# Kernel tuning notes

Measured on AMD Instinct MI355X. Metric: run time of the kernel, lower is better.

The kernel has to match this reference:

```python
import jax, jax.numpy as jnp
import numpy as np

B, T, I, H, O = 256, 512, 128, 256, 1


def setup_inputs() -> dict:
    key = jax.random.key(0)
    ks = jax.random.split(key, 7)
    s_ih = 1.0 / np.sqrt(H)
    return {
        "x": jax.random.normal(ks[0], (B, T, I), dtype=jnp.float32),
        "W_ih": jax.random.uniform(ks[1], (H, I), jnp.float32, -s_ih, s_ih),
        "W_hh": jax.random.uniform(ks[2], (H, H), jnp.float32, -s_ih, s_ih),
        "b_ih": jax.random.uniform(ks[3], (H,), jnp.float32, -s_ih, s_ih),
        "b_hh": jax.random.uniform(ks[4], (H,), jnp.float32, -s_ih, s_ih),
        "fc_w": jax.random.uniform(ks[5], (O, H), jnp.float32, -s_ih, s_ih),
        "fc_b": jax.random.uniform(ks[6], (O,), jnp.float32, -s_ih, s_ih),
    }


def reference(x, W_ih, W_hh, b_ih, b_hh, fc_w, fc_b):
    # Elman RNN (tanh), batch_first, single layer, h0 = zeros.
    # Only the last hidden state feeds the fc head, so scan carries h only.
    b = b_ih + b_hh
    xW = jnp.einsum('bti,hi->tbh', x, W_ih) + b  # precompute input projection [T,B,H]

    def step(h, xw_t):
        h = jnp.tanh(xw_t + h @ W_hh.T)
        return h, None

    h0 = jnp.zeros((x.shape[0], W_hh.shape[0]), dtype=x.dtype)
    h_last, _ = jax.lax.scan(step, h0, xW)
    return h_last @ fc_w.T + fc_b  # [B, O]
```

## Files before the change

kernel.cpp:

```cpp
#include <hip/hip_runtime.h>
#include <hip/hip_bf16.h>

#define B_ 256
#define T_ 512
#define I_ 128
#define H_ 256

typedef __bf16 bf16x8 __attribute__((ext_vector_type(8)));
typedef float  f32x4  __attribute__((ext_vector_type(4)));
typedef unsigned short u16;
typedef unsigned int   u32;

union U16x8Cast { uint4 v; bf16x8 b; };

__device__ inline u16 f2b(float f) {
    union { __bf16 h; u16 u; } c; c.h = (__bf16)f; return c.u;
}
__device__ inline bf16x8 pack8(float4 lo, float4 hi) {
    bf16x8 f;
    f[0]=(__bf16)lo.x; f[1]=(__bf16)lo.y; f[2]=(__bf16)lo.z; f[3]=(__bf16)lo.w;
    f[4]=(__bf16)hi.x; f[5]=(__bf16)hi.y; f[6]=(__bf16)hi.z; f[7]=(__bf16)hi.w;
    return f;
}
__device__ inline uint2 pack4(float a, float b, float c, float d) {
    uint2 p;
    p.x = (u32)f2b(a) | ((u32)f2b(b) << 16);
    p.y = (u32)f2b(c) | ((u32)f2b(d) << 16);
    return p;
}
__device__ inline f32x4 b4_to_f32x4(uint2 u) {
    f32x4 r;
    r[0] = __uint_as_float(u.x << 16);
    r[1] = __uint_as_float(u.x & 0xFFFF0000u);
    r[2] = __uint_as_float(u.y << 16);
    r[3] = __uint_as_float(u.y & 0xFFFF0000u);
    return r;
}
__device__ inline float fast_tanh(float x) {
    float e = __expf(2.f * x);
    float d = 1.f + e;
    float r;
    asm("v_rcp_f32 %0, %1" : "=v"(r) : "v"(d));
    return fmaf(-2.f, r, 1.f);
}

#define WG_BARRIER() asm volatile("s_waitcnt lgkmcnt(0)\n\ts_barrier" ::: "memory")

#define LDST 264
__global__ __launch_bounds__(256, 2) void xw_gemm_mfma(const float* __restrict__ x,
                                                       const float* __restrict__ W_ih,
                                                       const float* __restrict__ b_ih,
                                                       const float* __restrict__ b_hh,
                                                       u16* __restrict__ xw) {
    __shared__ u16 tile[64 * LDST];

    const int tid  = (int)threadIdx.x;
    const int wave = tid >> 6;
    const int lane = tid & 63;
    const int q    = lane >> 4;
    const int ml   = lane & 15;
    const int m0   = (int)blockIdx.x * 128;
    const int b    = m0 >> 9;
    const int t0   = m0 & 511;
    const int n0   = wave * 64;

    bf16x8 wA[4][4];
#pragma unroll
    for (int tau = 0; tau < 4; ++tau) {
        const float* wr = W_ih + (size_t)(n0 + tau * 16 + ml) * I_;
#pragma unroll
        for (int kap = 0; kap < 4; ++kap) {
            const int k0 = kap * 32 + q * 8;
            wA[tau][kap] = pack8(*(const float4*)(wr + k0), *(const float4*)(wr + k0 + 4));
        }
    }

    f32x4 acc[8][4];
#pragma unroll
    for (int mt = 0; mt < 8; ++mt)
#pragma unroll
        for (int tau = 0; tau < 4; ++tau) acc[mt][tau] = (f32x4)0.f;

#pragma unroll
    for (int kap = 0; kap < 4; ++kap) {
        bf16x8 xB[8];
#pragma unroll
        for (int mt = 0; mt < 8; ++mt) {
            const float* xr = x + (size_t)(m0 + mt * 16 + ml) * I_ + kap * 32 + q * 8;
            xB[mt] = pack8(*(const float4*)xr, *(const float4*)(xr + 4));
        }
#pragma unroll
        for (int mt = 0; mt < 8; ++mt)
#pragma unroll
            for (int tau = 0; tau < 4; ++tau)
                acc[mt][tau] = __builtin_amdgcn_mfma_f32_16x16x32_bf16(
                    wA[tau][kap], xB[mt], acc[mt][tau], 0, 0, 0);
    }

    float4 bias4[4];
#pragma unroll
    for (int tau = 0; tau < 4; ++tau) {
        const int n = n0 + tau * 16 + q * 4;
        float4 bi = *(const float4*)(b_ih + n);
        float4 bh = *(const float4*)(b_hh + n);
        bias4[tau] = make_float4(bi.x + bh.x, bi.y + bh.y, bi.z + bh.z, bi.w + bh.w);
    }

#pragma unroll
    for (int p = 0; p < 2; ++p) {
        if (p) __syncthreads();
#pragma unroll
        for (int mt = 0; mt < 4; ++mt) {
            const int row = mt * 16 + ml;
            const int mg  = p * 4 + mt;
#pragma unroll
            for (int tau = 0; tau < 4; ++tau) {
                uint2 pk = pack4(acc[mg][tau][0] + bias4[tau].x,
                                 acc[mg][tau][1] + bias4[tau].y,
                                 acc[mg][tau][2] + bias4[tau].z,
                                 acc[mg][tau][3] + bias4[tau].w);
                *(uint2*)(tile + row * LDST + n0 + tau * 16 + q * 4) = pk;
            }
        }
        __syncthreads();
#pragma unroll
        for (int s = 0; s < 4; ++s) {
            const int rr = s * 16 + (tid >> 4);
            const int c  = tid & 15;
            const uint4* srcp = (const uint4*)(tile + rr * LDST);
            uint4* dstp = (uint4*)(xw + ((size_t)(t0 + p * 64 + rr) * B_ + b) * H_);
            uint4 v0 = srcp[c];
            uint4 v1 = srcp[c + 16];
            dstp[c] = v0;
            dstp[c + 16] = v1;
        }
    }
}

__global__ __launch_bounds__(512, 2) void rnn_scan_mfma(const u16* __restrict__ xw,
                                                        const float* __restrict__ W_hh,
                                                        const float* __restrict__ fc_w,
                                                        const float* __restrict__ fc_b,
                                                        float* __restrict__ out) {
    __shared__ __attribute__((aligned(16))) u16 hbuf[2][4096];
    __shared__ float red[8][16];

    const int tid  = (int)threadIdx.x;
    const int wave = tid >> 6;
    const int lane = tid & 63;
    const int q    = lane >> 4;
    const int m    = lane & 15;
    const int b0   = (int)blockIdx.x * 16;

    bf16x8 wf[2][8];
#pragma unroll
    for (int tau2 = 0; tau2 < 2; ++tau2) {
        const float* wr = W_hh + (size_t)(wave * 32 + tau2 * 16 + m) * H_;
#pragma unroll
        for (int kap = 0; kap < 8; ++kap) {
            const int k0 = kap * 32 + q * 8;
            wf[tau2][kap] = pack8(*(const float4*)(wr + k0), *(const float4*)(wr + k0 + 4));
        }
    }

    int widx[2];
#pragma unroll
    for (int tau2 = 0; tau2 < 2; ++tau2) {
        const int nbw = wave * 32 + tau2 * 16 + q * 4;
        widx[tau2] = (nbw >> 5) * 512 + (((nbw >> 3) & 3) * 16 + m) * 8 + (nbw & 7);
    }

    {
        uint4* p = (uint4*)&hbuf[0][0];
        const uint4 z = {0u, 0u, 0u, 0u};
        p[tid] = z;
    }
    WG_BARRIER();

    const u16* xwp = xw + (size_t)(b0 + m) * H_ + (wave * 32 + q * 4);
    const size_t tstride = (size_t)B_ * H_;

    uint2 pfA[2], pfB[2];
    pfA[0] = *(const uint2*)(xwp);
    pfA[1] = *(const uint2*)(xwp + 16);
    pfB[0] = *(const uint2*)(xwp + tstride);
    pfB[1] = *(const uint2*)(xwp + tstride + 16);

    int cur = 0;
    f32x4 acc[2];
    for (int tt = 0; tt < T_ / 2; ++tt) {
        {
            const int t = 2 * tt;
            acc[0] = b4_to_f32x4(pfA[0]);
            acc[1] = b4_to_f32x4(pfA[1]);
            if (t + 2 < T_) {
                const u16* pt = xwp + (size_t)(t + 2) * tstride;
                pfA[0] = *(const uint2*)(pt);
                pfA[1] = *(const uint2*)(pt + 16);
            }
            const uint4* hb = (const uint4*)&hbuf[cur][0];
#pragma unroll
            for (int kap = 0; kap < 8; ++kap) {
                U16x8Cast c; c.v = hb[kap * 64 + lane];
                acc[0] = __builtin_amdgcn_mfma_f32_16x16x32_bf16(wf[0][kap], c.b, acc[0], 0, 0, 0);
                acc[1] = __builtin_amdgcn_mfma_f32_16x16x32_bf16(wf[1][kap], c.b, acc[1], 0, 0, 0);
            }
            u16* wb = &hbuf[cur ^ 1][0];
#pragma unroll
            for (int tau2 = 0; tau2 < 2; ++tau2) {
                uint2 pk = pack4(fast_tanh(acc[tau2][0]), fast_tanh(acc[tau2][1]),
                                 fast_tanh(acc[tau2][2]), fast_tanh(acc[tau2][3]));
                *(uint2*)(wb + widx[tau2]) = pk;
            }
            WG_BARRIER();
            cur ^= 1;
        }
        {
            const int t = 2 * tt + 1;
            acc[0] = b4_to_f32x4(pfB[0]);
            acc[1] = b4_to_f32x4(pfB[1]);
            if (t + 2 < T_) {
                const u16* pt = xwp + (size_t)(t + 2) * tstride;
                pfB[0] = *(const uint2*)(pt);
                pfB[1] = *(const uint2*)(pt + 16);
            }
            const uint4* hb = (const uint4*)&hbuf[cur][0];
#pragma unroll
            for (int kap = 0; kap < 8; ++kap) {
                U16x8Cast c; c.v = hb[kap * 64 + lane];
                acc[0] = __builtin_amdgcn_mfma_f32_16x16x32_bf16(wf[0][kap], c.b, acc[0], 0, 0, 0);
                acc[1] = __builtin_amdgcn_mfma_f32_16x16x32_bf16(wf[1][kap], c.b, acc[1], 0, 0, 0);
            }
            if (t != T_ - 1) {
                u16* wb = &hbuf[cur ^ 1][0];
#pragma unroll
                for (int tau2 = 0; tau2 < 2; ++tau2) {
                    uint2 pk = pack4(fast_tanh(acc[tau2][0]), fast_tanh(acc[tau2][1]),
                                     fast_tanh(acc[tau2][2]), fast_tanh(acc[tau2][3]));
                    *(uint2*)(wb + widx[tau2]) = pk;
                }
                WG_BARRIER();
                cur ^= 1;
            }
        }
    }

    float4 fcw[2];
#pragma unroll
    for (int tau2 = 0; tau2 < 2; ++tau2)
        fcw[tau2] = *(const float4*)(fc_w + wave * 32 + tau2 * 16 + q * 4);

    float partial = 0.f;
#pragma unroll
    for (int tau2 = 0; tau2 < 2; ++tau2) {
        partial += fast_tanh(acc[tau2][0]) * fcw[tau2].x;
        partial += fast_tanh(acc[tau2][1]) * fcw[tau2].y;
        partial += fast_tanh(acc[tau2][2]) * fcw[tau2].z;
        partial += fast_tanh(acc[tau2][3]) * fcw[tau2].w;
    }
    partial += __shfl_xor(partial, 16);
    partial += __shfl_xor(partial, 32);
    __syncthreads();
    if (lane < 16) red[wave][m] = partial;
    __syncthreads();
    if (tid < 16) {
        float s = red[0][tid] + red[1][tid] + red[2][tid] + red[3][tid]
                + red[4][tid] + red[5][tid] + red[6][tid] + red[7][tid];
        out[b0 + tid] = s + fc_b[0];
    }
}

extern "C" void kernel_launch(void* const* d_in, const int* in_sizes, int n_in,
                              void* d_out, int out_size, void* d_ws, size_t ws_size,
                              hipStream_t stream) {
    const float* x    = (const float*)d_in[0];
    const float* W_ih = (const float*)d_in[1];
    const float* W_hh = (const float*)d_in[2];
    const float* b_ih = (const float*)d_in[3];
    const float* b_hh = (const float*)d_in[4];
    const float* fc_w = (const float*)d_in[5];
    const float* fc_b = (const float*)d_in[6];
    float* out = (float*)d_out;

    u16* xwbuf = (u16*)d_ws;
    xw_gemm_mfma<<<(B_ * T_) / 128, 256, 0, stream>>>(x, W_ih, b_ih, b_hh, xwbuf);
    rnn_scan_mfma<<<B_ / 16, 512, 0, stream>>>(xwbuf, W_hh, fc_w, fc_b, out);
}
```

Measured before the change: 457.9 us.

## Halve scan workgroup to 4 waves, each computing 64 hidden units

The recurrent scan kernel now uses 256 threads (4 waves) per 16-batch block instead of 512, and each wave owns 64 hidden outputs with four accumulator tiles and four W_hh fragment sets held in registers. This cuts the per-step barrier cost and the number of waves synchronising, and gives each wave more independent MFMA chains to hide latency. In exchange each wave does twice the MFMA and tanh work per step on the serial critical path, and register pressure roughly doubles.

Result: slower. 531.3 us (+16.0%).

```diff
diff --git a/kernel.cpp b/kernel.cpp
--- a/kernel.cpp
+++ b/kernel.cpp
@@ -137,13 +137,13 @@
     }
 }
 
-__global__ __launch_bounds__(512, 2) void rnn_scan_mfma(const u16* __restrict__ xw,
+__global__ __launch_bounds__(256, 1) void rnn_scan_mfma(const u16* __restrict__ xw,
                                                         const float* __restrict__ W_hh,
                                                         const float* __restrict__ fc_w,
                                                         const float* __restrict__ fc_b,
                                                         float* __restrict__ out) {
     __shared__ __attribute__((aligned(16))) u16 hbuf[2][4096];
-    __shared__ float red[8][16];
+    __shared__ float red[4][16];
 
     const int tid  = (int)threadIdx.x;
     const int wave = tid >> 6;
@@ -152,92 +152,97 @@
     const int m    = lane & 15;
     const int b0   = (int)blockIdx.x * 16;
 
-    bf16x8 wf[2][8];
-#pragma unroll
-    for (int tau2 = 0; tau2 < 2; ++tau2) {
-        const float* wr = W_hh + (size_t)(wave * 32 + tau2 * 16 + m) * H_;
+    bf16x8 wf[4][8];
+#pragma unroll
+    for (int tau = 0; tau < 4; ++tau) {
+        const float* wr = W_hh + (size_t)(wave * 64 + tau * 16 + m) * H_;
 #pragma unroll
         for (int kap = 0; kap < 8; ++kap) {
             const int k0 = kap * 32 + q * 8;
-            wf[tau2][kap] = pack8(*(const float4*)(wr + k0), *(const float4*)(wr + k0 + 4));
-        }
-    }
-
-    int widx[2];
-#pragma unroll
-    for (int tau2 = 0; tau2 < 2; ++tau2) {
-        const int nbw = wave * 32 + tau2 * 16 + q * 4;
-        widx[tau2] = (nbw >> 5) * 512 + (((nbw >> 3) & 3) * 16 + m) * 8 + (nbw & 7);
+            wf[tau][kap] = pack8(*(const float4*)(wr + k0), *(const float4*)(wr + k0 + 4));
+        }
+    }
+
+    int widx[4];
+#pragma unroll
+    for (int tau = 0; tau < 4; ++tau) {
+        const int nbw = wave * 64 + tau * 16 + q * 4;
+        widx[tau] = (nbw >> 5) * 512 + (((nbw >> 3) & 3) * 16 + m) * 8 + (nbw & 7);
     }
 
     {
         uint4* p = (uint4*)&hbuf[0][0];
         const uint4 z = {0u, 0u, 0u, 0u};
-        p[tid] = z;
+        p[tid] = z; p[tid + 256] = z;
     }
     WG_BARRIER();
 
-    const u16* xwp = xw + (size_t)(b0 + m) * H_ + (wave * 32 + q * 4);
+    const u16* xwp = xw + (size_t)(b0 + m) * H_ + (wave * 64 + q * 4);
     const size_t tstride = (size_t)B_ * H_;
 
-    uint2 pfA[2], pfB[2];
-    pfA[0] = *(const uint2*)(xwp);
-    pfA[1] = *(const uint2*)(xwp + 16);
-    pfB[0] = *(const uint2*)(xwp + tstride);
-    pfB[1] = *(const uint2*)(xwp + tstride + 16);
+    uint2 pfA[4], pfB[4];
+#pragma unroll
+    for (int tau = 0; tau < 4; ++tau) {
+        pfA[tau] = *(const uint2*)(xwp + tau * 16);
+        pfB[tau] = *(const uint2*)(xwp + tstride + tau * 16);
+    }
 
     int cur = 0;
-    f32x4 acc[2];
+    f32x4 acc[4];
     for (int tt = 0; tt < T_ / 2; ++tt) {
         {
             const int t = 2 * tt;
-            acc[0] = b4_to_f32x4(pfA[0]);
-            acc[1] = b4_to_f32x4(pfA[1]);
+#pragma unroll
+            for (int tau = 0; tau < 4; ++tau) acc[tau] = b4_to_f32x4(pfA[tau]);
             if (t + 2 < T_) {
                 const u16* pt = xwp + (size_t)(t + 2) * tstride;
-                pfA[0] = *(const uint2*)(pt);
-                pfA[1] = *(const uint2*)(pt + 16);
+#pragma unroll
+                for (int tau = 0; tau < 4; ++tau) pfA[tau] = *(const uint2*)(pt + tau * 16);
             }
             const uint4* hb = (const uint4*)&hbuf[cur][0];
 #pragma unroll
             for (int kap = 0; kap < 8; ++kap) {
                 U16x8Cast c; c.v = hb[kap * 64 + lane];
-                acc[0] = __builtin_amdgcn_mfma_f32_16x16x32_bf16(wf[0][kap], c.b, acc[0], 0, 0, 0);
-                acc[1] = __builtin_amdgcn_mfma_f32_16x16x32_bf16(wf[1][kap], c.b, acc[1], 0, 0, 0);
+#pragma unroll
+                for (int tau = 0; tau < 4; ++tau)
+                    acc[tau] = __builtin_amdgcn_mfma_f32_16x16x32_bf16(
+                        wf[tau][kap], c.b, acc[tau], 0, 0, 0);
             }
             u16* wb = &hbuf[cur ^ 1][0];
 #pragma unroll
-            for (int tau2 = 0; tau2 < 2; ++tau2) {
-                uint2 pk = pack4(fast_tanh(acc[tau2][0]), fast_tanh(acc[tau2][1]),
-                                 fast_tanh(acc[tau2][2]), fast_tanh(acc[tau2][3]));
-                *(uint2*)(wb + widx[tau2]) = pk;
+            for (int tau = 0; tau < 4; ++tau) {
+                uint2 pk = pack4(fast_tanh(acc[tau][0]), fast_tanh(acc[tau][1]),
+                                 fast_tanh(acc[tau][2]), fast_tanh(acc[tau][3]));
+                *(uint2*)(wb + widx[tau]) = pk;
             }
             WG_BARRIER();
             cur ^= 1;
         }
         {
             const int t = 2 * tt + 1;
-            acc[0] = b4_to_f32x4(pfB[0]);
-            acc[1] = b4_to_f32x4(pfB[1]);
+#pragma unroll
+            for (int tau = 0; tau < 4; ++tau) acc[tau] = b4_to_f32x4(pfB[tau]);
             if (t + 2 < T_) {
                 const u16* pt = xwp + (size_t)(t + 2) * tstride;
-                pfB[0] = *(const uint2*)(pt);
-                pfB[1] = *(const uint2*)(pt + 16);
+#pragma unroll
+                for (int tau = 0; tau < 4; ++tau) pfB[tau] = *(const uint2*)(pt + tau * 16);
             }
             const uint4* hb = (const uint4*)&hbuf[cur][0];
 #pragma unroll
             for (int kap = 0; kap < 8; ++kap) {
                 U16x8Cast c; c.v = hb[kap * 64 + lane];
-                acc[0] = __builtin_amdgcn_mfma_f32_16x16x32_bf16(wf[0][kap], c.b, acc[0], 0, 0, 0);
-                acc[1] = __builtin_amdgcn_mfma_f32_16x16x32_bf16(wf[1][kap], c.b, acc[1], 0, 0, 0);
+#pragma unroll
+                for (int tau = 0; tau < 4; ++tau)
+                    acc[tau] = __builtin_amdgcn_mfma_f32_16x16x32_bf16(
+                        wf[tau][kap], c.b, acc[tau], 0, 0, 0);
             }
             if (t != T_ - 1) {
                 u16* wb = &hbuf[cur ^ 1][0];
 #pragma unroll
-                for (int tau2 = 0; tau2 < 2; ++tau2) {
-                    uint2 pk = pack4(fast_tanh(acc[tau2][0]), fast_tanh(acc[tau2][1]),
-                                     fast_tanh(acc[tau2][2]), fast_tanh(acc[tau2][3]));
-                    *(uint2*)(wb + widx[tau2]) = pk;
+                for (int tau = 0; tau < 4; ++tau) {
+                    uint2 pk = pack4(fast_tanh(acc[tau][0]), fast_tanh(acc[tau][1]),
+                                     fast_tanh(acc[tau][2]), fast_tanh(acc[tau][3]));
+                    *(uint2*)(wb + widx[tau]) = pk;
                 }
                 WG_BARRIER();
                 cur ^= 1;
@@ -245,29 +250,26 @@
         }
     }
 
-    float4 fcw[2];
-#pragma unroll
-    for (int tau2 = 0; tau2 < 2; ++tau2)
-        fcw[tau2] = *(const float4*)(fc_w + wave * 32 + tau2 * 16 + q * 4);
+    float4 fcw[4];
+#pragma unroll
+    for (int tau = 0; tau < 4; ++tau)
+        fcw[tau] = *(const float4*)(fc_w + wave * 64 + tau * 16 + q * 4);
 
     float partial = 0.f;
 #pragma unroll
-    for (int tau2 = 0; tau2 < 2; ++tau2) {
-        partial += fast_tanh(acc[tau2][0]) * fcw[tau2].x;
-        partial += fast_tanh(acc[tau2][1]) * fcw[tau2].y;
-        partial += fast_tanh(acc[tau2][2]) * fcw[tau2].z;
-        partial += fast_tanh(acc[tau2][3]) * fcw[tau2].w;
+    for (int tau = 0; tau < 4; ++tau) {
+        partial += fast_tanh(acc[tau][0]) * fcw[tau].x;
+        partial += fast_tanh(acc[tau][1]) * fcw[tau].y;
+        partial += fast_tanh(acc[tau][2]) * fcw[tau].z;
+        partial += fast_tanh(acc[tau][3]) * fcw[tau].w;
     }
     partial += __shfl_xor(partial, 16);
     partial += __shfl_xor(partial, 32);
     __syncthreads();
     if (lane < 16) red[wave][m] = partial;
     __syncthreads();
-    if (tid < 16) {
-        float s = red[0][tid] + red[1][tid] + red[2][tid] + red[3][tid]
-                + red[4][tid] + red[5][tid] + red[6][tid] + red[7][tid];
-        out[b0 + tid] = s + fc_b[0];
-    }
+    if (tid < 16)
+        out[b0 + tid] = red[0][tid] + red[1][tid] + red[2][tid] + red[3][tid] + fc_b[0];
 }
 
 extern "C" void kernel_launch(void* const* d_in, const int* in_sizes, int n_in,
@@ -284,5 +286,5 @@
 
     u16* xwbuf = (u16*)d_ws;
     xw_gemm_mfma<<<(B_ * T_) / 128, 256, 0, stream>>>(x, W_ih, b_ih, b_hh, xwbuf);
-    rnn_scan_mfma<<<B_ / 16, 512, 0, stream>>>(xwbuf, W_hh, fc_w, fc_b, out);
-}
+    rnn_scan_mfma<<<B_ / 16, 256, 0, stream>>>(xwbuf, W_hh, fc_w, fc_b, out);
+}
```
